# Kernel optimization log

Measured on AMD Instinct MI355X. Metric: run time of the kernel, lower is better.

Reference implementation:

```python
import jax, jax.numpy as jnp
import numpy as np

B, SEED, GEN = 32, 128, 384
IN, H, OUT = 171, 1024, 171


def setup_inputs() -> dict:
    key = jax.random.key(0)
    ks = jax.random.split(key, 16)
    s = 0.05
    w = lambda k, shape: (jax.random.normal(k, shape, jnp.float32) * s)
    inp = {
        "seed_seq": jax.random.normal(ks[0], (B, SEED, IN), jnp.float32),
        "Wih1": w(ks[1], (4 * H, IN)),  "Whh1": w(ks[2], (4 * H, H)),
        "bih1": w(ks[3], (4 * H,)),     "bhh1": w(ks[4], (4 * H,)),
        "Wih2": w(ks[5], (4 * H, H)),   "Whh2": w(ks[6], (4 * H, H)),
        "bih2": w(ks[7], (4 * H,)),     "bhh2": w(ks[8], (4 * H,)),
        "Wih3": w(ks[9], (4 * H, H)),   "Whh3": w(ks[10], (4 * H, H)),
        "bih3": w(ks[11], (4 * H,)),    "bhh3": w(ks[12], (4 * H,)),
        "Wdec": w(ks[13], (OUT, H)),    "bdec": w(ks[14], (OUT,)),
        "gen_len": GEN,
    }
    return inp


def _lstm_cell(x, h, c, Wih, Whh, bih, bhh):
    # PyTorch LSTMCell: gate order i, f, g, o
    gates = x @ Wih.T + bih + h @ Whh.T + bhh  # [B, 4H]
    i, f, g, o = jnp.split(gates, 4, axis=-1)
    c_new = jax.nn.sigmoid(f) * c + jax.nn.sigmoid(i) * jnp.tanh(g)
    h_new = jax.nn.sigmoid(o) * jnp.tanh(c_new)
    return h_new, c_new


def reference(seed_seq, Wih1, Whh1, bih1, bhh1, Wih2, Whh2, bih2, bhh2,
              Wih3, Whh3, bih3, bhh3, Wdec, bdec, gen_len):
    batch = seed_seq.shape[0]
    hsz = Whh1.shape[1]
    z = jnp.zeros((batch, hsz), seed_seq.dtype)

    def step(state, x):
        h1, c1, h2, c2, h3, c3 = state
        h1, c1 = _lstm_cell(x, h1, c1, Wih1, Whh1, bih1, bhh1)
        h2, c2 = _lstm_cell(h1, h2, c2, Wih2, Whh2, bih2, bhh2)
        h3, c3 = _lstm_cell(h2, h3, c3, Wih3, Whh3, bih3, bhh3)
        out = h3 @ Wdec.T + bdec
        return (h1, c1, h2, c2, h3, c3), out

    # conditioning (seed) phase: scan over time-major seed sequence
    state0 = (z, z, z, z, z, z)
    state, seed_outs = jax.lax.scan(step, state0, jnp.swapaxes(seed_seq, 0, 1))

    def gen_step(carry, _):
        cur, st = carry
        st, out = step(st, cur)
        return (out, st), out

    _, gen_outs = jax.lax.scan(gen_step, (seed_outs[-1], state), None, length=gen_len)

    outs = jnp.concatenate([seed_outs, gen_outs], axis=0)  # [T, B, OUT]
    return jnp.swapaxes(outs, 0, 1)  # [B, T, OUT]
```

## Files before the change

### kernel.cpp

```cpp
#include <hip/hip_runtime.h>
#include <hip/hip_bf16.h>
#include <math.h>

#define NB    32
#define NSEED 128
#define NTT   512
#define NIN   171
#define NINP  192
#define NH    1024
#define NG    4096
#define NOUT  171
#define NOUTP 176
#define NWG   256

typedef unsigned short u16;
typedef unsigned int u32;
typedef __attribute__((ext_vector_type(8))) short bf16x8;
typedef __attribute__((ext_vector_type(4))) float f32x4;
typedef __attribute__((ext_vector_type(4))) int i32x4;

__device__ __host__ inline u16 f2bf(float x) {
  union { float f; unsigned u; } v; v.f = x;
  unsigned r = v.u + 0x7FFFu + ((v.u >> 16) & 1u);
  return (u16)(r >> 16);
}

__global__ void pack_mat(const float* __restrict__ src, u16* __restrict__ dst, int ktiles) {
  int id = blockIdx.x * 256 + threadIdx.x;
  int total = ktiles * 256 * 64;
  if (id >= total) return;
  int lane = id & 63;
  int nt = (id >> 6) & 255;
  int kt = id >> 14;
  int c = lane & 15, q = lane >> 4;
  int r = (c & 3) * 1024 + nt * 4 + (c >> 2);
  int K = ktiles * 32;
  const float* s = src + (size_t)r * K + kt * 32 + q * 8;
  __attribute__((aligned(16))) u16 o[8];
#pragma unroll
  for (int j = 0; j < 8; ++j) o[j] = f2bf(s[j]);
  *(bf16x8*)(dst + (size_t)id * 8) = *(const bf16x8*)o;
}

__global__ void pack_wih1(const float* __restrict__ src, u16* __restrict__ dst) {
  int id = blockIdx.x * 256 + threadIdx.x;
  if (id >= 6 * 256 * 64) return;
  int lane = id & 63;
  int nt = (id >> 6) & 255;
  int kt = id >> 14;
  int c = lane & 15, q = lane >> 4;
  int r = (c & 3) * 1024 + nt * 4 + (c >> 2);
  int k0 = kt * 32 + q * 8;
  __attribute__((aligned(16))) u16 o[8];
#pragma unroll
  for (int j = 0; j < 8; ++j) {
    int k = k0 + j;
    o[j] = (k < NIN) ? f2bf(src[(size_t)r * NIN + k]) : (u16)0;
  }
  *(bf16x8*)(dst + (size_t)id * 8) = *(const bf16x8*)o;
}

__global__ void pack_wdec(const float* __restrict__ src, u16* __restrict__ dst) {
  int id = blockIdx.x * 256 + threadIdx.x;
  if (id >= 32 * 11 * 64) return;
  int lane = id & 63;
  int nt = (id >> 6) % 11;
  int kt = (id >> 6) / 11;
  int c = lane & 15, q = lane >> 4;
  int r = nt * 16 + c;
  int k0 = kt * 32 + q * 8;
  __attribute__((aligned(16))) u16 o[8];
#pragma unroll
  for (int j = 0; j < 8; ++j) {
    o[j] = (r < NOUT) ? f2bf(src[(size_t)r * NH + k0 + j]) : (u16)0;
  }
  *(bf16x8*)(dst + (size_t)id * 8) = *(const bf16x8*)o;
}

__global__ void pack_seed(const float* __restrict__ src, u16* __restrict__ dst) {
  int id = blockIdx.x * 256 + threadIdx.x;
  if (id >= NSEED * NB * NINP) return;
  int kp = id % NINP;
  int b = (id / NINP) % NB;
  int t = id / (NINP * NB);
  float v = (kp < NIN) ? src[((size_t)b * NSEED + t) * NIN + kp] : 0.f;
  dst[id] = f2bf(v);
}

__global__ void wfuse_kernel(const float* __restrict__ wih1, const float* __restrict__ wdec,
                             float* __restrict__ tmp) {
  int n = blockIdx.x;
  int k = blockIdx.y * 256 + threadIdx.x;
  const float* wr = wih1 + (size_t)n * NIN;
  float s = 0.f;
  for (int i = 0; i < NIN; ++i) s += wr[i] * wdec[(size_t)i * NH + k];
  tmp[(size_t)n * NH + k] = s;
}

__global__ void prep_bias(const float* bih1, const float* bhh1, const float* bih2, const float* bhh2,
                          const float* bih3, const float* bhh3, const float* __restrict__ wih1,
                          const float* __restrict__ bdec_in,
                          float* b1s, float* b1g, float* b2, float* b3, float* bdecp,
                          int* __restrict__ flags) {
  int n = blockIdx.x * 256 + threadIdx.x;
  if (n >= NG) return;
  int wgi = n >> 4, c = n & 15;
  int r = (c & 3) * 1024 + wgi * 4 + (c >> 2);
  float v1 = bih1[r] + bhh1[r];
  b1s[n] = v1;
  float bf = 0.f;
  for (int i = 0; i < NIN; ++i) bf += wih1[(size_t)r * NIN + i] * bdec_in[i];
  b1g[n] = v1 + bf;
  b2[n] = bih2[r] + bhh2[r];
  b3[n] = bih3[r] + bhh3[r];
  if (n < NOUTP) bdecp[n] = (n < NOUT) ? bdec_in[n] : 0.f;
  if (n < NWG) flags[n] = 0;
}

__device__ __forceinline__ float fsig(float x) {
  return __builtin_amdgcn_rcpf(1.f + __expf(-x));
}
__device__ __forceinline__ float ftanh(float x) {
  return 1.f - 2.f * __builtin_amdgcn_rcpf(1.f + __expf(2.f * x));
}

#define MFMA_BF16 __builtin_amdgcn_mfma_f32_16x16x32_bf16

__device__ __forceinline__ void mm32_lds(f32x4& d0, f32x4& d1, const u16* wl,
                                         const u16* __restrict__ x, int wv, int lane) {
  int m = lane & 15, q = lane >> 4;
  const u16* xa = x + m * NH + q * 8 + wv * 32;
  const u16* xb = xa + 16 * NH;
  const u16* wb = wl + lane * 8;
  bf16x8 w[8], a0[8], a1[8];
#pragma unroll
  for (int i = 0; i < 8; ++i) {
    a0[i] = *(const bf16x8*)(xa + i * 128);
    a1[i] = *(const bf16x8*)(xb + i * 128);
  }
#pragma unroll
  for (int i = 0; i < 8; ++i) w[i] = *(const bf16x8*)(wb + (size_t)(wv + 4 * i) * 512);
#pragma unroll
  for (int i = 0; i < 8; ++i) {
    d0 = MFMA_BF16(a0[i], w[i], d0, 0, 0, 0);
    d1 = MFMA_BF16(a1[i], w[i], d1, 0, 0, 0);
  }
}

__device__ __forceinline__ void mm32_glb(f32x4& d0, f32x4& d1, const u16* __restrict__ wgb,
                                         const u16* __restrict__ x, int wv, int lane) {
  int m = lane & 15, q = lane >> 4;
  const u16* xa = x + m * NH + q * 8 + wv * 32;
  const u16* xb = xa + 16 * NH;
  const u16* wb = wgb + lane * 8;
  bf16x8 w[8], a0[8], a1[8];
#pragma unroll
  for (int i = 0; i < 8; ++i) {
    a0[i] = *(const bf16x8*)(xa + i * 128);
    a1[i] = *(const bf16x8*)(xb + i * 128);
  }
#pragma unroll
  for (int i = 0; i < 8; ++i) w[i] = *(const bf16x8*)(wb + (size_t)(wv + 4 * i) * 131072);
#pragma unroll
  for (int i = 0; i < 8; ++i) {
    d0 = MFMA_BF16(a0[i], w[i], d0, 0, 0, 0);
    d1 = MFMA_BF16(a1[i], w[i], d1, 0, 0, 0);
  }
}

__device__ __forceinline__ void mm6_glb(f32x4& d0, f32x4& d1, const u16* __restrict__ wbase,
                                        const u16* __restrict__ x, int wv, int lane) {
  int m = lane & 15, q = lane >> 4;
  const u16* xa = x + m * NINP + q * 8;
  const u16* xb = xa + 16 * NINP;
  const u16* wb = wbase + lane * 8;
#pragma unroll
  for (int i = 0; i < 2; ++i) {
    int kt = wv + 4 * i;
    if (kt >= 6) break;
    bf16x8 w = *(const bf16x8*)(wb + (size_t)kt * 131072);
    bf16x8 a0 = *(const bf16x8*)(xa + kt * 32);
    bf16x8 a1 = *(const bf16x8*)(xb + kt * 32);
    d0 = MFMA_BF16(a0, w, d0, 0, 0, 0);
    d1 = MFMA_BF16(a1, w, d1, 0, 0, 0);
  }
}

__global__ __launch_bounds__(256, 1) void lstm_main(
    const u16* __restrict__ whh1, const u16* __restrict__ whh2, const u16* __restrict__ whh3,
    const u16* __restrict__ wih2, const u16* __restrict__ wih3,
    const u16* __restrict__ wfuse, const u16* __restrict__ wih1,
    const u16* __restrict__ seedp,
    u16* __restrict__ h1h, u16* __restrict__ h2h, u16* __restrict__ h3h,
    const float* __restrict__ b1s, const float* __restrict__ b1g,
    const float* __restrict__ b2, const float* __restrict__ b3,
    int* __restrict__ flags)
{
  __shared__ u16  wlds[4 * 16384];
  __shared__ float red[4][64][8];
  __shared__ float biasLds[4][16];
  __shared__ float cst[3][32][4];

  int wg = blockIdx.x;
  int tid = threadIdx.x;
  int wv = tid >> 6, lane = tid & 63;

  {
    const u16* srcs[4] = { wih2 + (size_t)wg * 512, wih3 + (size_t)wg * 512,
                           wfuse + (size_t)wg * 512, whh1 + (size_t)wg * 512 };
#pragma unroll
    for (int m = 0; m < 4; ++m) {
      for (int i = tid; i < 2048; i += 256) {
        int kt = i >> 6, ln = i & 63;
        *(bf16x8*)&wlds[m * 16384 + (kt * 64 + ln) * 8] =
            *(const bf16x8*)(srcs[m] + ((size_t)kt * 16384 + ln) * 8);
      }
    }
    float* cp = &cst[0][0][0];
    for (int i = tid; i < 3 * 32 * 4; i += 256) cp[i] = 0.f;
    if (tid < 64) {
      int row = tid >> 4, c = tid & 15;
      const float* src = (row == 0) ? b1s : (row == 1) ? b1g : (row == 2) ? b2 : b3;
      biasLds[row][c] = src[wg * 16 + c];
    }
  }
  __syncthreads();

  const u16* whh2g = whh2 + (size_t)wg * 512;
  const u16* whh3g = whh3 + (size_t)wg * 512;
  const u16* wih1g = wih1 + (size_t)wg * 512;

  int ep = 0;
  for (int t = 0; t < NTT; ++t) {
    for (int l = 0; l < 3; ++l) {
      f32x4 d0 = {0.f, 0.f, 0.f, 0.f}, d1 = {0.f, 0.f, 0.f, 0.f};
      bool isseed = (t < NSEED);

      if (l == 0 && isseed)
        mm6_glb(d0, d1, wih1g, seedp + (size_t)t * NB * NINP, wv, lane);
      if (t > 0) {
        if (l == 0)
          mm32_lds(d0, d1, &wlds[3 * 16384], h1h + (size_t)(t - 1) * NB * NH, wv, lane);
        else if (l == 1)
          mm32_glb(d0, d1, whh2g, h2h + (size_t)(t - 1) * NB * NH, wv, lane);
        else
          mm32_glb(d0, d1, whh3g, h3h + (size_t)(t - 1) * NB * NH, wv, lane);
      }

      bool skipwait = (l == 0 && isseed);
      if (ep > 0 && !skipwait && wv == 1) {
        const int* fp = flags + (lane << 2);
        for (;;) {
          i32x4 f;
          asm volatile("global_load_dwordx4 %0, %1, off sc0 sc1\n\ts_waitcnt vmcnt(0)"
                       : "=v"(f) : "v"(fp) : "memory");
          int mn = min(min(f.x, f.y), min(f.z, f.w));
          if (__all(mn >= ep)) break;
          __builtin_amdgcn_s_sleep(1);
        }
      }
      __syncthreads();

      if (l == 0) {
        if (!isseed)
          mm32_lds(d0, d1, &wlds[2 * 16384], h3h + (size_t)(t - 1) * NB * NH, wv, lane);
      } else {
        const u16* xs = (l == 1) ? h1h + (size_t)t * NB * NH
                                 : h2h + (size_t)t * NB * NH;
        mm32_lds(d0, d1, &wlds[(l - 1) * 16384], xs, wv, lane);
      }

#pragma unroll
      for (int r = 0; r < 4; ++r) { red[wv][lane][r] = d0[r]; red[wv][lane][4 + r] = d1[r]; }
      __syncthreads();

      int epn = ep + 1;
      if (tid < 64) {
        __builtin_amdgcn_s_setprio(1);
        int b = tid & 31, upair = tid >> 5;
        int srcl_base = ((b & 15) >> 2) << 4;
        int idx = ((b >> 4) << 2) | (b & 3);
        int bsel = (l == 0) ? (isseed ? 0 : 1) : (l + 1);
        float g[8];
#pragma unroll
        for (int u2 = 0; u2 < 2; ++u2) {
          int u = upair * 2 + u2;
#pragma unroll
          for (int gi = 0; gi < 4; ++gi) {
            int c = u * 4 + gi;
            int srcl = srcl_base | c;
            g[u2 * 4 + gi] = red[0][srcl][idx] + red[1][srcl][idx] +
                             red[2][srcl][idx] + red[3][srcl][idx] + biasLds[bsel][c];
          }
        }
        unsigned hv[2];
#pragma unroll
        for (int u2 = 0; u2 < 2; ++u2) {
          int u = upair * 2 + u2;
          float si = fsig(g[u2 * 4 + 0]);
          float sf = fsig(g[u2 * 4 + 1]);
          float so = fsig(g[u2 * 4 + 3]);
          float cn = sf * cst[l][b][u] + si * ftanh(g[u2 * 4 + 2]);
          cst[l][b][u] = cn;
          hv[u2] = (unsigned)f2bf(so * ftanh(cn));
        }
        unsigned val = hv[0] | (hv[1] << 16);
        u16* hdst = (l == 0) ? h1h + (size_t)t * NB * NH
                  : (l == 1) ? h2h + (size_t)t * NB * NH
                             : h3h + (size_t)t * NB * NH;
        u32* hp = (u32*)hdst + (size_t)b * 512 + wg * 2 + upair;
        __hip_atomic_store(hp, val, __ATOMIC_RELAXED, __HIP_MEMORY_SCOPE_AGENT);
        asm volatile("s_waitcnt vmcnt(0)" ::: "memory");
        if (tid == 0)
          __hip_atomic_store(&flags[wg], epn, __ATOMIC_RELAXED, __HIP_MEMORY_SCOPE_AGENT);
        __builtin_amdgcn_s_setprio(0);
      }
      ep = epn;
    }
  }
}

__global__ __launch_bounds__(256) void dec_kernel(
    const u16* __restrict__ h3h, const u16* __restrict__ wdec,
    const float* __restrict__ bdecp, float* __restrict__ out)
{
  int task = blockIdx.x * 4 + (threadIdx.x >> 6);
  int lane = threadIdx.x & 63;
  int nt = task % 11, rt = task / 11;
  if (rt >= NTT) return;
  int m = lane & 15, q = lane >> 4;
  const u16* xa = h3h + ((size_t)rt * 32 + m) * NH + q * 8;
  const u16* xb = xa + (size_t)16 * NH;
  f32x4 d0 = {0.f, 0.f, 0.f, 0.f}, d1 = {0.f, 0.f, 0.f, 0.f};
  for (int kt = 0; kt < 32; ++kt) {
    bf16x8 bf = *(const bf16x8*)(wdec + ((size_t)(kt * 11 + nt) * 64 + lane) * 8);
    bf16x8 a0 = *(const bf16x8*)(xa + kt * 32);
    bf16x8 a1 = *(const bf16x8*)(xb + kt * 32);
    d0 = MFMA_BF16(a0, bf, d0, 0, 0, 0);
    d1 = MFMA_BF16(a1, bf, d1, 0, 0, 0);
  }
  int o = nt * 16 + m;
  if (o >= NOUT) return;
  float bv = bdecp[o];
#pragma unroll
  for (int reg = 0; reg < 4; ++reg) {
    int row0 = rt * 32 + q * 4 + reg;
    out[(((size_t)(row0 & 31)) * NTT + (row0 >> 5)) * NOUT + o] = d0[reg] + bv;
    int row1 = row0 + 16;
    out[(((size_t)(row1 & 31)) * NTT + (row1 >> 5)) * NOUT + o] = d1[reg] + bv;
  }
}

extern "C" void kernel_launch(void* const* d_in, const int* in_sizes, int n_in,
                              void* d_out, int out_size, void* d_ws, size_t ws_size,
                              hipStream_t stream) {
  const float* seed = (const float*)d_in[0];
  const float* Wih1 = (const float*)d_in[1];
  const float* Whh1 = (const float*)d_in[2];
  const float* bih1 = (const float*)d_in[3];
  const float* bhh1 = (const float*)d_in[4];
  const float* Wih2 = (const float*)d_in[5];
  const float* Whh2 = (const float*)d_in[6];
  const float* bih2 = (const float*)d_in[7];
  const float* bhh2 = (const float*)d_in[8];
  const float* Wih3 = (const float*)d_in[9];
  const float* Whh3 = (const float*)d_in[10];
  const float* bih3 = (const float*)d_in[11];
  const float* bhh3 = (const float*)d_in[12];
  const float* Wdec = (const float*)d_in[13];
  const float* bdec = (const float*)d_in[14];

  char* ws = (char*)d_ws;
  size_t off = 0;
  auto alloc = [&](size_t bytes) -> void* {
    void* p = ws + off;
    off += (bytes + 63) & ~(size_t)63;
    return p;
  };
  const size_t BIGPK = (size_t)32 * 256 * 64 * 8 * 2;
  const size_t HHIST = (size_t)NTT * NB * NH * 2;
  u16* whh1p  = (u16*)alloc(BIGPK);
  u16* whh2p  = (u16*)alloc(BIGPK);
  u16* whh3p  = (u16*)alloc(BIGPK);
  u16* wih2p  = (u16*)alloc(BIGPK);
  u16* wih3p  = (u16*)alloc(BIGPK);
  u16* wfusep = (u16*)alloc(BIGPK);
  u16* wih1p  = (u16*)alloc((size_t)6 * 256 * 64 * 8 * 2);
  u16* wdecp  = (u16*)alloc((size_t)32 * 11 * 64 * 8 * 2);
  u16* seedp  = (u16*)alloc((size_t)NSEED * NB * NINP * 2);
  u16* h1h    = (u16*)alloc(HHIST);
  u16* h2h    = (u16*)alloc(HHIST);
  u16* h3h    = (u16*)alloc(HHIST);
  float* b1s  = (float*)alloc((size_t)NG * 4);
  float* b1g  = (float*)alloc((size_t)NG * 4);
  float* b2   = (float*)alloc((size_t)NG * 4);
  float* b3   = (float*)alloc((size_t)NG * 4);
  float* bdecp = (float*)alloc((size_t)NOUTP * 4);
  int* flags  = (int*)alloc((size_t)NWG * 4);
  float* wftmp = (float*)h3h;

  pack_mat<<<dim3(2048), dim3(256), 0, stream>>>(Whh1, whh1p, 32);
  pack_mat<<<dim3(2048), dim3(256), 0, stream>>>(Whh2, whh2p, 32);
  pack_mat<<<dim3(2048), dim3(256), 0, stream>>>(Whh3, whh3p, 32);
  pack_mat<<<dim3(2048), dim3(256), 0, stream>>>(Wih2, wih2p, 32);
  pack_mat<<<dim3(2048), dim3(256), 0, stream>>>(Wih3, wih3p, 32);
  pack_wih1<<<dim3(384), dim3(256), 0, stream>>>(Wih1, wih1p);
  wfuse_kernel<<<dim3(4096, 4), dim3(256), 0, stream>>>(Wih1, Wdec, wftmp);
  pack_mat<<<dim3(2048), dim3(256), 0, stream>>>(wftmp, wfusep, 32);
  pack_wdec<<<dim3(88), dim3(256), 0, stream>>>(Wdec, wdecp);
  pack_seed<<<dim3(3072), dim3(256), 0, stream>>>(seed, seedp);
  prep_bias<<<dim3(16), dim3(256), 0, stream>>>(bih1, bhh1, bih2, bhh2, bih3, bhh3,
                                                Wih1, bdec, b1s, b1g, b2, b3, bdecp, flags);
  lstm_main<<<dim3(NWG), dim3(256), 0, stream>>>(
      whh1p, whh2p, whh3p, wih2p, wih3p, wfusep, wih1p, seedp,
      h1h, h2h, h3h, b1s, b1g, b2, b3, flags);
  dec_kernel<<<dim3(1408), dim3(256), 0, stream>>>(h3h, wdecp, bdecp, (float*)d_out);
}
```

Before: 6.708 ms.

## Replace per-workgroup flag barrier with poisoned-value polling on hidden states

Removes the flag array and the spin on epoch counters. The hidden-state history is instead pre-filled with a sentinel bf16 pattern, and each wave polls its own input fragments with cache-bypassing loads until no sentinel remains. This drops the store-then-flag round trip and the dedicated polling wave, letting data arrival itself signal readiness. It risks a false wait if a real computed value equals the sentinel (bf16 2.0, which sigmoid*tanh cannot produce), and it adds an extra kernel to poison the whole history buffer.

```diff
diff --git a/kernel.cpp b/kernel.cpp
--- a/kernel.cpp
+++ b/kernel.cpp
@@ -18,6 +18,8 @@
 typedef __attribute__((ext_vector_type(8))) short bf16x8;
 typedef __attribute__((ext_vector_type(4))) float f32x4;
 typedef __attribute__((ext_vector_type(4))) int i32x4;
+
+#define PZ32 0x40004000u
 
 __device__ __host__ inline u16 f2bf(float x) {
   union { float f; unsigned u; } v; v.f = x;
@@ -97,11 +99,16 @@
   tmp[(size_t)n * NH + k] = s;
 }
 
+__global__ void poison_h(u32* __restrict__ p) {
+  size_t id = (size_t)blockIdx.x * 256 + threadIdx.x;
+  i32x4 v = { (int)PZ32, (int)PZ32, (int)PZ32, (int)PZ32 };
+  ((i32x4*)p)[id] = v;
+}
+
 __global__ void prep_bias(const float* bih1, const float* bhh1, const float* bih2, const float* bhh2,
                           const float* bih3, const float* bhh3, const float* __restrict__ wih1,
                           const float* __restrict__ bdec_in,
-                          float* b1s, float* b1g, float* b2, float* b3, float* bdecp,
-                          int* __restrict__ flags) {
+                          float* b1s, float* b1g, float* b2, float* b3, float* bdecp) {
   int n = blockIdx.x * 256 + threadIdx.x;
   if (n >= NG) return;
   int wgi = n >> 4, c = n & 15;
@@ -114,7 +121,6 @@
   b2[n] = bih2[r] + bhh2[r];
   b3[n] = bih3[r] + bhh3[r];
   if (n < NOUTP) bdecp[n] = (n < NOUT) ? bdec_in[n] : 0.f;
-  if (n < NWG) flags[n] = 0;
 }
 
 __device__ __forceinline__ float fsig(float x) {
@@ -126,45 +132,81 @@
 
 #define MFMA_BF16 __builtin_amdgcn_mfma_f32_16x16x32_bf16
 
-__device__ __forceinline__ void mm32_lds(f32x4& d0, f32x4& d1, const u16* wl,
-                                         const u16* __restrict__ x, int wv, int lane) {
+__device__ __forceinline__ bf16x8 asbf(i32x4 v) {
+  union { i32x4 i; bf16x8 b; } u; u.i = v; return u.b;
+}
+
+__device__ __forceinline__ u32 zh(u32 x) {
+  x ^= PZ32;
+  return (x - 0x00010001u) & ~x & 0x80008000u;
+}
+__device__ __forceinline__ int fragbad(i32x4 v) {
+  return (zh((u32)v.x) | zh((u32)v.y) | zh((u32)v.z) | zh((u32)v.w)) != 0;
+}
+
+__device__ __forceinline__ void sc_x(const u16* __restrict__ x, int wv, int lane,
+                                     i32x4 (&v0)[8], i32x4 (&v1)[8]) {
   int m = lane & 15, q = lane >> 4;
   const u16* xa = x + m * NH + q * 8 + wv * 32;
   const u16* xb = xa + 16 * NH;
-  const u16* wb = wl + lane * 8;
-  bf16x8 w[8], a0[8], a1[8];
 #pragma unroll
   for (int i = 0; i < 8; ++i) {
-    a0[i] = *(const bf16x8*)(xa + i * 128);
-    a1[i] = *(const bf16x8*)(xb + i * 128);
-  }
-#pragma unroll
-  for (int i = 0; i < 8; ++i) w[i] = *(const bf16x8*)(wb + (size_t)(wv + 4 * i) * 512);
-#pragma unroll
-  for (int i = 0; i < 8; ++i) {
-    d0 = MFMA_BF16(a0[i], w[i], d0, 0, 0, 0);
-    d1 = MFMA_BF16(a1[i], w[i], d1, 0, 0, 0);
-  }
-}
-
-__device__ __forceinline__ void mm32_glb(f32x4& d0, f32x4& d1, const u16* __restrict__ wgb,
-                                         const u16* __restrict__ x, int wv, int lane) {
+    asm volatile("global_load_dwordx4 %0, %1, off sc0 sc1" : "=v"(v0[i]) : "v"(xa + i * 128));
+    asm volatile("global_load_dwordx4 %0, %1, off sc0 sc1" : "=v"(v1[i]) : "v"(xb + i * 128));
+  }
+  asm volatile("s_waitcnt vmcnt(0)" ::: "memory");
+}
+
+__device__ __forceinline__ void poll_x(const u16* __restrict__ x, int wv, int lane,
+                                       i32x4 (&v0)[8], i32x4 (&v1)[8]) {
   int m = lane & 15, q = lane >> 4;
   const u16* xa = x + m * NH + q * 8 + wv * 32;
   const u16* xb = xa + 16 * NH;
+#pragma unroll
+  for (int i = 0; i < 8; ++i) {
+    asm volatile("global_load_dwordx4 %0, %1, off sc0 sc1" : "=v"(v0[i]) : "v"(xa + i * 128));
+    asm volatile("global_load_dwordx4 %0, %1, off sc0 sc1" : "=v"(v1[i]) : "v"(xb + i * 128));
+  }
+  asm volatile("s_waitcnt vmcnt(0)" ::: "memory");
+  for (;;) {
+    int bad = 0;
+#pragma unroll
+    for (int i = 0; i < 8; ++i) {
+      if (fragbad(v0[i])) bad |= (1 << i);
+      if (fragbad(v1[i])) bad |= (1 << (8 + i));
+    }
+    if (!__any(bad)) break;
+    __builtin_amdgcn_s_sleep(1);
+#pragma unroll
+    for (int i = 0; i < 8; ++i) {
+      if (bad & (1 << i))
+        asm volatile("global_load_dwordx4 %0, %1, off sc0 sc1" : "=v"(v0[i]) : "v"(xa + i * 128));
+      if (bad & (1 << (8 + i)))
+        asm volatile("global_load_dwordx4 %0, %1, off sc0 sc1" : "=v"(v1[i]) : "v"(xb + i * 128));
+    }
+    asm volatile("s_waitcnt vmcnt(0)" ::: "memory");
+  }
+}
+
+__device__ __forceinline__ void mm_w_lds(f32x4& d0, f32x4& d1, const u16* wl, int wv, int lane,
+                                         const i32x4 (&v0)[8], const i32x4 (&v1)[8]) {
+  const u16* wb = wl + lane * 8;
+#pragma unroll
+  for (int i = 0; i < 8; ++i) {
+    bf16x8 w = *(const bf16x8*)(wb + (size_t)(wv + 4 * i) * 512);
+    d0 = MFMA_BF16(asbf(v0[i]), w, d0, 0, 0, 0);
+    d1 = MFMA_BF16(asbf(v1[i]), w, d1, 0, 0, 0);
+  }
+}
+__device__ __forceinline__ void mm_w_glb(f32x4& d0, f32x4& d1, const u16* __restrict__ wgb,
+                                         int wv, int lane,
+                                         const i32x4 (&v0)[8], const i32x4 (&v1)[8]) {
   const u16* wb = wgb + lane * 8;
-  bf16x8 w[8], a0[8], a1[8];
 #pragma unroll
   for (int i = 0; i < 8; ++i) {
-    a0[i] = *(const bf16x8*)(xa + i * 128);
-    a1[i] = *(const bf16x8*)(xb + i * 128);
-  }
-#pragma unroll
-  for (int i = 0; i < 8; ++i) w[i] = *(const bf16x8*)(wb + (size_t)(wv + 4 * i) * 131072);
-#pragma unroll
-  for (int i = 0; i < 8; ++i) {
-    d0 = MFMA_BF16(a0[i], w[i], d0, 0, 0, 0);
-    d1 = MFMA_BF16(a1[i], w[i], d1, 0, 0, 0);
+    bf16x8 w = *(const bf16x8*)(wb + (size_t)(wv + 4 * i) * 131072);
+    d0 = MFMA_BF16(asbf(v0[i]), w, d0, 0, 0, 0);
+    d1 = MFMA_BF16(asbf(v1[i]), w, d1, 0, 0, 0);
   }
 }
 
@@ -193,8 +235,7 @@
     const u16* __restrict__ seedp,
     u16* __restrict__ h1h, u16* __restrict__ h2h, u16* __restrict__ h3h,
     const float* __restrict__ b1s, const float* __restrict__ b1g,
-    const float* __restrict__ b2, const float* __restrict__ b3,
-    int* __restrict__ flags)
+    const float* __restrict__ b2, const float* __restrict__ b3)
 {
   __shared__ u16  wlds[4 * 16384];
   __shared__ float red[4][64][8];
@@ -230,51 +271,47 @@
   const u16* whh3g = whh3 + (size_t)wg * 512;
   const u16* wih1g = wih1 + (size_t)wg * 512;
 
-  int ep = 0;
   for (int t = 0; t < NTT; ++t) {
     for (int l = 0; l < 3; ++l) {
+      bool isseed = (t < NSEED);
+      bool skipfresh = (l == 0 && isseed);
+
       f32x4 d0 = {0.f, 0.f, 0.f, 0.f}, d1 = {0.f, 0.f, 0.f, 0.f};
-      bool isseed = (t < NSEED);
 
       if (l == 0 && isseed)
         mm6_glb(d0, d1, wih1g, seedp + (size_t)t * NB * NINP, wv, lane);
       if (t > 0) {
-        if (l == 0)
-          mm32_lds(d0, d1, &wlds[3 * 16384], h1h + (size_t)(t - 1) * NB * NH, wv, lane);
-        else if (l == 1)
-          mm32_glb(d0, d1, whh2g, h2h + (size_t)(t - 1) * NB * NH, wv, lane);
-        else
-          mm32_glb(d0, d1, whh3g, h3h + (size_t)(t - 1) * NB * NH, wv, lane);
-      }
-
-      bool skipwait = (l == 0 && isseed);
-      if (ep > 0 && !skipwait && wv == 1) {
-        const int* fp = flags + (lane << 2);
-        for (;;) {
-          i32x4 f;
-          asm volatile("global_load_dwordx4 %0, %1, off sc0 sc1\n\ts_waitcnt vmcnt(0)"
-                       : "=v"(f) : "v"(fp) : "memory");
-          int mn = min(min(f.x, f.y), min(f.z, f.w));
-          if (__all(mn >= ep)) break;
-          __builtin_amdgcn_s_sleep(1);
+        i32x4 v0[8], v1[8];
+        if (l == 0) {
+          sc_x(h1h + (size_t)(t - 1) * NB * NH, wv, lane, v0, v1);
+          mm_w_lds(d0, d1, &wlds[3 * 16384], wv, lane, v0, v1);
+        } else if (l == 1) {
+          sc_x(h2h + (size_t)(t - 1) * NB * NH, wv, lane, v0, v1);
+          mm_w_glb(d0, d1, whh2g, wv, lane, v0, v1);
+        } else {
+          sc_x(h3h + (size_t)(t - 1) * NB * NH, wv, lane, v0, v1);
+          mm_w_glb(d0, d1, whh3g, wv, lane, v0, v1);
         }
       }
+
       __syncthreads();
 
-      if (l == 0) {
-        if (!isseed)
-          mm32_lds(d0, d1, &wlds[2 * 16384], h3h + (size_t)(t - 1) * NB * NH, wv, lane);
-      } else {
-        const u16* xs = (l == 1) ? h1h + (size_t)t * NB * NH
-                                 : h2h + (size_t)t * NB * NH;
-        mm32_lds(d0, d1, &wlds[(l - 1) * 16384], xs, wv, lane);
+      if (!skipfresh) {
+        i32x4 v0[8], v1[8];
+        const u16* xfr = (l == 0) ? h3h + (size_t)(t - 1) * NB * NH
+                       : (l == 1) ? h1h + (size_t)t * NB * NH
+                                  : h2h + (size_t)t * NB * NH;
+        poll_x(xfr, wv, lane, v0, v1);
+        const u16* wfr = (l == 0) ? &wlds[2 * 16384]
+                       : (l == 1) ? &wlds[0]
+                                  : &wlds[1 * 16384];
+        mm_w_lds(d0, d1, wfr, wv, lane, v0, v1);
       }
 
 #pragma unroll
       for (int r = 0; r < 4; ++r) { red[wv][lane][r] = d0[r]; red[wv][lane][4 + r] = d1[r]; }
       __syncthreads();
 
-      int epn = ep + 1;
       if (tid < 64) {
         __builtin_amdgcn_s_setprio(1);
         int b = tid & 31, upair = tid >> 5;
@@ -283,16 +320,14 @@
         int bsel = (l == 0) ? (isseed ? 0 : 1) : (l + 1);
         float g[8];
 #pragma unroll
-        for (int u2 = 0; u2 < 2; ++u2) {
-          int u = upair * 2 + u2;
+        for (int u2 = 0; u2 < 2; ++u2)
 #pragma unroll
           for (int gi = 0; gi < 4; ++gi) {
-            int c = u * 4 + gi;
+            int c = (upair * 2 + u2) * 4 + gi;
             int srcl = srcl_base | c;
             g[u2 * 4 + gi] = red[0][srcl][idx] + red[1][srcl][idx] +
                              red[2][srcl][idx] + red[3][srcl][idx] + biasLds[bsel][c];
           }
-        }
         unsigned hv[2];
 #pragma unroll
         for (int u2 = 0; u2 < 2; ++u2) {
@@ -310,12 +345,8 @@
                              : h3h + (size_t)t * NB * NH;
         u32* hp = (u32*)hdst + (size_t)b * 512 + wg * 2 + upair;
         __hip_atomic_store(hp, val, __ATOMIC_RELAXED, __HIP_MEMORY_SCOPE_AGENT);
-        asm volatile("s_waitcnt vmcnt(0)" ::: "memory");
-        if (tid == 0)
-          __hip_atomic_store(&flags[wg], epn, __ATOMIC_RELAXED, __HIP_MEMORY_SCOPE_AGENT);
         __builtin_amdgcn_s_setprio(0);
       }
-      ep = epn;
     }
   }
 }
@@ -396,7 +427,6 @@
   float* b2   = (float*)alloc((size_t)NG * 4);
   float* b3   = (float*)alloc((size_t)NG * 4);
   float* bdecp = (float*)alloc((size_t)NOUTP * 4);
-  int* flags  = (int*)alloc((size_t)NWG * 4);
   float* wftmp = (float*)h3h;
 
   pack_mat<<<dim3(2048), dim3(256), 0, stream>>>(Whh1, whh1p, 32);
@@ -407,12 +437,13 @@
   pack_wih1<<<dim3(384), dim3(256), 0, stream>>>(Wih1, wih1p);
   wfuse_kernel<<<dim3(4096, 4), dim3(256), 0, stream>>>(Wih1, Wdec, wftmp);
   pack_mat<<<dim3(2048), dim3(256), 0, stream>>>(wftmp, wfusep, 32);
+  poison_h<<<dim3(24576), dim3(256), 0, stream>>>((u32*)h1h);
   pack_wdec<<<dim3(88), dim3(256), 0, stream>>>(Wdec, wdecp);
   pack_seed<<<dim3(3072), dim3(256), 0, stream>>>(seed, seedp);
   prep_bias<<<dim3(16), dim3(256), 0, stream>>>(bih1, bhh1, bih2, bhh2, bih3, bhh3,
-                                                Wih1, bdec, b1s, b1g, b2, b3, bdecp, flags);
+                                                Wih1, bdec, b1s, b1g, b2, b3, bdecp);
   lstm_main<<<dim3(NWG), dim3(256), 0, stream>>>(
       whh1p, whh2p, whh3p, wih2p, wih3p, wfusep, wih1p, seedp,
-      h1h, h2h, h3h, b1s, b1g, b2, b3, flags);
+      h1h, h2h, h3h, b1s, b1g, b2, b3);
   dec_kernel<<<dim3(1408), dim3(256), 0, stream>>>(h3h, wdecp, bdecp, (float*)d_out);
 }
```

Result: slower. 8.230 ms (+22.7%).
